# Optimization experiments

Hardware: AMD Instinct MI355X
Metric: run time of the kernel (lower is better)

## Reference

```python
import jax, jax.numpy as jnp
import numpy as np
import math

D_SINGLE, D_PAIR, H, PQ, PV = 384, 128, 12, 4, 8
DH = D_SINGLE // H
OUT_DIM = H * DH + H * PV * 4 + H * D_PAIR


def setup_inputs() -> dict:
    key = jax.random.key(0)
    ks = jax.random.split(key, 24)
    B, L = 1, 512
    inp = {
        'single': jax.random.normal(ks[0], (B, L, D_SINGLE), jnp.float32),
        'pair': jax.random.normal(ks[1], (B, L, L, D_PAIR), jnp.float32),
        'rot_mats': jax.random.normal(ks[2], (B, L, 3, 3), jnp.float32),
        'trans': jax.random.normal(ks[3], (B, L, 3), jnp.float32),
        'mask': jnp.ones((B, L), jnp.float32),
        'ln_w': jnp.ones((D_SINGLE,), jnp.float32),
        'ln_b': jnp.zeros((D_SINGLE,), jnp.float32),
        'Wq': jax.random.normal(ks[4], (D_SINGLE, H * DH), jnp.float32) * 0.02,
        'bq': jnp.zeros((H * DH,), jnp.float32),
        'Wk': jax.random.normal(ks[5], (D_SINGLE, H * DH), jnp.float32) * 0.02,
        'bk': jnp.zeros((H * DH,), jnp.float32),
        'Wv': jax.random.normal(ks[6], (D_SINGLE, H * DH), jnp.float32) * 0.02,
        'bv': jnp.zeros((H * DH,), jnp.float32),
        'Wqp': jax.random.normal(ks[7], (D_SINGLE, H * PQ * 3), jnp.float32) * 0.02,
        'bqp': jnp.zeros((H * PQ * 3,), jnp.float32),
        'Wkp': jax.random.normal(ks[8], (D_SINGLE, H * PQ * 3), jnp.float32) * 0.02,
        'bkp': jnp.zeros((H * PQ * 3,), jnp.float32),
        'Wvp': jax.random.normal(ks[9], (D_SINGLE, H * PV * 3), jnp.float32) * 0.02,
        'bvp': jnp.zeros((H * PV * 3,), jnp.float32),
        'Wpb': jax.random.normal(ks[10], (D_PAIR, H), jnp.float32) * 0.02,
        'bpb': jnp.zeros((H,), jnp.float32),
        'Wo': jax.random.normal(ks[11], (OUT_DIM, D_SINGLE), jnp.float32) * 0.02,
        'bo': jnp.zeros((D_SINGLE,), jnp.float32),
        'w_c': jnp.asarray(1.0 / math.sqrt(3.0), jnp.float32),
        'w_l': jnp.asarray(1.0 / 3.0, jnp.float32),
        'gamma_h': jnp.ones((H,), jnp.float32),
    }
    return inp


def _layer_norm(x, w, b, eps=1e-5):
    mu = jnp.mean(x, axis=-1, keepdims=True)
    var = jnp.mean((x - mu) ** 2, axis=-1, keepdims=True)
    return (x - mu) * jax.lax.rsqrt(var + eps) * w + b


def reference(single, pair, rot_mats, trans, mask, ln_w, ln_b, Wq, bq, Wk, bk, Wv, bv,
              Wqp, bqp, Wkp, bkp, Wvp, bvp, Wpb, bpb, Wo, bo, w_c, w_l, gamma_h):
    B, L, _ = single.shape
    sn = _layer_norm(single, ln_w, ln_b)
    q = (sn @ Wq + bq).reshape(B, L, H, DH)
    k = (sn @ Wk + bk).reshape(B, L, H, DH)
    v = (sn @ Wv + bv).reshape(B, L, H, DH)
    qp = (sn @ Wqp + bqp).reshape(B, L, H, PQ, 3)
    kp = (sn @ Wkp + bkp).reshape(B, L, H, PQ, 3)
    vp = (sn @ Wvp + bvp).reshape(B, L, H, PV, 3)

    t = trans[:, :, None, None, :]  # [B,L,1,1,3]
    qg = jnp.einsum('blij,blhpj->blhpi', rot_mats, qp) + t
    kg = jnp.einsum('blij,blhpj->blhpi', rot_mats, kp) + t
    vg = jnp.einsum('blij,blhpj->blhpi', rot_mats, vp) + t

    # sequence logits [B,H,L,L]
    seq_logits = jnp.einsum('bihd,bjhd->bhij', q, k) * w_c / math.sqrt(DH)

    # geometric logits: pairwise point distances [B,H,L,L]
    q_pts = jnp.transpose(qg, (0, 2, 1, 3, 4))  # [B,H,L,PQ,3]
    k_pts = jnp.transpose(kg, (0, 2, 1, 3, 4))
    diff = q_pts[:, :, :, None] - k_pts[:, :, None]  # [B,H,L,L,PQ,3]
    dist_sq = jnp.sum(diff ** 2, axis=-1)            # [B,H,L,L,PQ]
    geo_logits = -0.5 * jnp.sum(dist_sq, axis=-1) * gamma_h[None, :, None, None] * w_l

    pair_bias = jnp.transpose(pair @ Wpb + bpb, (0, 3, 1, 2))  # [B,H,L,L]
    logits = seq_logits + geo_logits + pair_bias

    mask_2d = (mask[:, :, None] * mask[:, None, :])[:, None]  # [B,1,L,L]
    logits = jnp.where(mask_2d > 0, logits, jnp.float32(-1e9))
    attn = jax.nn.softmax(logits, axis=-1)  # [B,H,L,L]

    # sequence aggregation -> [B,L,H,DH]
    seq_out = jnp.einsum('bhij,bjhd->bihd', attn, v).reshape(B, L, H * DH)

    # point aggregation -> local frame features
    pts_out = jnp.einsum('bhij,bjhpd->bihpd', attn, vg)  # [B,L,H,PV,3]
    pts_local = jnp.einsum('blji,blhpj->blhpi', rot_mats, pts_out - t)
    pts_norm = jnp.linalg.norm(pts_local, axis=-1, keepdims=True)
    pts_feat = jnp.concatenate([pts_norm, pts_local], axis=-1).reshape(B, L, H * PV * 4)

    # pair aggregation -> [B,L,H*D_PAIR]
    pair_out = jnp.einsum('bhij,bijd->bihd', attn, pair).reshape(B, L, H * D_PAIR)

    combined = jnp.concatenate([seq_out, pts_feat, pair_out], axis=-1)
    return combined @ Wo + bo
```

## Files before the change

kernel.cpp:

```cpp
#include <hip/hip_runtime.h>
#include <math.h>

#define LQ    512
#define DS    384
#define DPAIR 128
#define NH    12
#define NPP   1792
#define TJC   64
#define NC    8

typedef unsigned short u16;
typedef unsigned int   u32;
typedef __attribute__((ext_vector_type(8))) short bf16x8;
typedef __attribute__((ext_vector_type(4))) float f32x4;

__device__ inline u16 bf16_rne(float x) {
  u32 u = __float_as_uint(x);
  u32 r = (u + 0x7FFFu + ((u >> 16) & 1u)) >> 16;
  return (u16)r;
}
__device__ inline void split_bf16(float x, u16& h, u16& l) {
  u16 hb = bf16_rne(x);
  float hf = __uint_as_float(((u32)hb) << 16);
  h = hb;
  l = bf16_rne(x - hf);
}

__global__ __launch_bounds__(256) void k_prep(
    const float* __restrict__ Wq, const float* __restrict__ Wk,
    const float* __restrict__ Wv, const float* __restrict__ Wqp,
    const float* __restrict__ Wkp, const float* __restrict__ Wvp,
    const float* __restrict__ bq, const float* __restrict__ bk,
    const float* __restrict__ bv, const float* __restrict__ bqp,
    const float* __restrict__ bkp, const float* __restrict__ bvp,
    const float* __restrict__ Wpb, const float* __restrict__ Wo,
    const float* __restrict__ xs, const float* __restrict__ ln_w,
    const float* __restrict__ ln_b,
    u16* __restrict__ Wth, u16* __restrict__ Wtl,
    float* __restrict__ bcat, float* __restrict__ WpbT,
    u16* __restrict__ WoTh, u16* __restrict__ WoTl,
    u16* __restrict__ snh, u16* __restrict__ snl) {
  __shared__ u16 sh_hi[64][66], sh_lo[64][66];
  int blk = blockIdx.x, t = threadIdx.x;
  if (blk < 168) {
    int kb = blk / 28, cb = blk % 28;
    int k0 = kb * 64, c0 = cb * 64;
    for (int e = t; e < 4096; e += 256) {
      int rr = e >> 6, cc = e & 63;
      int k = k0 + rr, c = c0 + cc;
      float v = 0.f;
      if (c < 384)       v = Wq[k*384 + c];
      else if (c < 768)  v = Wk[k*384 + c-384];
      else if (c < 1152) v = Wv[k*384 + c-768];
      else if (c < 1296) v = Wqp[k*144 + c-1152];
      else if (c < 1440) v = Wkp[k*144 + c-1296];
      else if (c < 1728) v = Wvp[k*288 + c-1440];
      u16 h_, l_; split_bf16(v, h_, l_);
      sh_hi[rr][cc] = h_; sh_lo[rr][cc] = l_;
    }
    __syncthreads();
    for (int e = t; e < 4096; e += 256) {
      int cc = e >> 6, kk = e & 63;
      Wth[(size_t)(c0+cc)*DS + k0 + kk] = sh_hi[kk][cc];
      Wtl[(size_t)(c0+cc)*DS + k0 + kk] = sh_lo[kk][cc];
    }
  } else if (blk == 168) {
    for (int e = t; e < NPP + NH*DPAIR; e += 256) {
      if (e < NPP) {
        int c = e;
        float v = 0.f;
        if (c < 384)       v = bq[c];
        else if (c < 768)  v = bk[c-384];
        else if (c < 1152) v = bv[c-768];
        else if (c < 1296) v = bqp[c-1152];
        else if (c < 1440) v = bkp[c-1296];
        else if (c < 1728) v = bvp[c-1440];
        bcat[c] = v;
      } else {
        int e2 = e - NPP;
        int k = e2 / NH, h = e2 % NH;
        WpbT[h*DPAIR + k] = Wpb[e2];
      }
    }
  } else if (blk < 385) {
    int idx = blk - 169;
    int kt = idx % 36, nt = idx / 36;
    int k0 = kt * 64, n0 = nt * 64;
    for (int e = t; e < 4096; e += 256) {
      int rr = e >> 6, cc = e & 63;
      float v = Wo[(size_t)(k0+rr)*384 + n0 + cc];
      u16 h_, l_; split_bf16(v, h_, l_);
      sh_hi[rr][cc] = h_; sh_lo[rr][cc] = l_;
    }
    __syncthreads();
    for (int e = t; e < 4096; e += 256) {
      int cc = e >> 6, kk = e & 63;
      WoTh[(size_t)(n0+cc)*2304 + k0 + kk] = sh_hi[kk][cc];
      WoTl[(size_t)(n0+cc)*2304 + k0 + kk] = sh_lo[kk][cc];
    }
  } else {
    int i = blk - 385;
    float* red = (float*)&sh_hi[0][0];
    float a0 = xs[i*DS + t];
    float a1 = (t < 128) ? xs[i*DS + 256 + t] : 0.f;
    red[t] = a0 + a1; __syncthreads();
    for (int s = 128; s > 0; s >>= 1) { if (t < s) red[t] += red[t+s]; __syncthreads(); }
    float mu = red[0] * (1.f/384.f);
    __syncthreads();
    float d0 = a0 - mu, d1 = (t < 128) ? (a1 - mu) : 0.f;
    red[t] = d0*d0 + d1*d1; __syncthreads();
    for (int s = 128; s > 0; s >>= 1) { if (t < s) red[t] += red[t+s]; __syncthreads(); }
    float rstd = rsqrtf(red[0] * (1.f/384.f) + 1e-5f);
    u16 h_, l_;
    float y0 = d0*rstd*ln_w[t] + ln_b[t];
    split_bf16(y0, h_, l_); snh[i*DS + t] = h_; snl[i*DS + t] = l_;
    if (t < 128) {
      float y1 = d1*rstd*ln_w[256+t] + ln_b[256+t];
      split_bf16(y1, h_, l_); snh[i*DS + 256 + t] = h_; snl[i*DS + 256 + t] = l_;
    }
  }
}

__global__ __launch_bounds__(256) void k_gemm_mfma(
    const u16* __restrict__ Ah, const u16* __restrict__ Al,
    const u16* __restrict__ Bth, const u16* __restrict__ Btl,
    const float* __restrict__ bias, float* __restrict__ C,
    float* __restrict__ Cpart, int M, int N, int K) {
  int t = threadIdx.x;
  int lane = t & 63, wave = t >> 6;
  int wr = wave >> 1, wc = wave & 1;
  int i0 = blockIdx.y * 64 + wr * 32;
  int j0 = blockIdx.x * 64 + wc * 32;
  int KS = gridDim.z;
  int kper = K / KS;
  size_t kbeg = (size_t)blockIdx.z * kper;
  int lr = lane & 15, lk = (lane >> 4) << 3;

  const u16* a0h = Ah  + (size_t)(i0 + lr) * K + kbeg + lk;
  const u16* a1h = a0h + (size_t)16 * K;
  const u16* a0l = Al  + (size_t)(i0 + lr) * K + kbeg + lk;
  const u16* a1l = a0l + (size_t)16 * K;
  const u16* b0h = Bth + (size_t)(j0 + lr) * K + kbeg + lk;
  const u16* b1h = b0h + (size_t)16 * K;
  const u16* b0l = Btl + (size_t)(j0 + lr) * K + kbeg + lk;
  const u16* b1l = b0l + (size_t)16 * K;

  f32x4 c00 = {0.f,0.f,0.f,0.f}, c01 = c00, c10 = c00, c11 = c00;
  for (int k = 0; k < kper; k += 32) {
    bf16x8 A0h = *(const bf16x8*)(a0h + k);
    bf16x8 A1h = *(const bf16x8*)(a1h + k);
    bf16x8 B0h = *(const bf16x8*)(b0h + k);
    bf16x8 B1h = *(const bf16x8*)(b1h + k);
    bf16x8 A0l = *(const bf16x8*)(a0l + k);
    bf16x8 A1l = *(const bf16x8*)(a1l + k);
    bf16x8 B0l = *(const bf16x8*)(b0l + k);
    bf16x8 B1l = *(const bf16x8*)(b1l + k);
    c00 = __builtin_amdgcn_mfma_f32_16x16x32_bf16(A0h, B0h, c00, 0, 0, 0);
    c01 = __builtin_amdgcn_mfma_f32_16x16x32_bf16(A0h, B1h, c01, 0, 0, 0);
    c10 = __builtin_amdgcn_mfma_f32_16x16x32_bf16(A1h, B0h, c10, 0, 0, 0);
    c11 = __builtin_amdgcn_mfma_f32_16x16x32_bf16(A1h, B1h, c11, 0, 0, 0);
    c00 = __builtin_amdgcn_mfma_f32_16x16x32_bf16(A0h, B0l, c00, 0, 0, 0);
    c01 = __builtin_amdgcn_mfma_f32_16x16x32_bf16(A0h, B1l, c01, 0, 0, 0);
    c10 = __builtin_amdgcn_mfma_f32_16x16x32_bf16(A1h, B0l, c10, 0, 0, 0);
    c11 = __builtin_amdgcn_mfma_f32_16x16x32_bf16(A1h, B1l, c11, 0, 0, 0);
    c00 = __builtin_amdgcn_mfma_f32_16x16x32_bf16(A0l, B0h, c00, 0, 0, 0);
    c01 = __builtin_amdgcn_mfma_f32_16x16x32_bf16(A0l, B1h, c01, 0, 0, 0);
    c10 = __builtin_amdgcn_mfma_f32_16x16x32_bf16(A1l, B0h, c10, 0, 0, 0);
    c11 = __builtin_amdgcn_mfma_f32_16x16x32_bf16(A1l, B1h, c11, 0, 0, 0);
  }

  int orow = (lane >> 4) << 2;
  int col0 = j0 + lr, col1 = j0 + 16 + lr;
  if (KS == 1) {
    float bb0 = bias[col0], bb1 = bias[col1];
    #pragma unroll
    for (int r = 0; r < 4; r++) {
      int row0 = i0 + orow + r, row1 = row0 + 16;
      C[(size_t)row0*N + col0] = c00[r] + bb0;
      C[(size_t)row0*N + col1] = c01[r] + bb1;
      C[(size_t)row1*N + col0] = c10[r] + bb0;
      C[(size_t)row1*N + col1] = c11[r] + bb1;
    }
  } else {
    float* dst = Cpart + (size_t)blockIdx.z * M * N;
    #pragma unroll
    for (int r = 0; r < 4; r++) {
      int row0 = i0 + orow + r, row1 = row0 + 16;
      dst[(size_t)row0*N + col0] = c00[r];
      dst[(size_t)row0*N + col1] = c01[r];
      dst[(size_t)row1*N + col0] = c10[r];
      dst[(size_t)row1*N + col1] = c11[r];
    }
  }
}

__global__ void k_reduce_bias(const float* __restrict__ part, const float* __restrict__ bias,
                              float* __restrict__ out, int MN, int N, int KS) {
  int e = blockIdx.x * 256 + threadIdx.x;
  if (e >= MN) return;
  float s = bias[e % N];
  for (int z = 0; z < KS; z++) s += part[(size_t)z*MN + e];
  out[e] = s;
}

__global__ __launch_bounds__(256) void k_feat_logits(
    const float* __restrict__ C1, const float* __restrict__ rot,
    const float* __restrict__ trans, const float* __restrict__ gamma,
    const float* __restrict__ w_c, const float* __restrict__ w_l,
    float* __restrict__ S) {
  __shared__ u16 Ash[64][72], Asl[64][72], Bsh[64][72], Bsl[64][72];
  int h = blockIdx.z;
  int i0 = blockIdx.y * 64, j0 = blockIdx.x * 64;
  int t = threadIdx.x;

  if (t < 128) {
    int row = t & 63, side = t >> 6;
    int gi = (side ? j0 : i0) + row;
    float R[9], tr[3];
    #pragma unroll
    for (int r = 0; r < 9; r++) R[r] = rot[(size_t)gi*9 + r];
    #pragma unroll
    for (int r = 0; r < 3; r++) tr[r] = trans[(size_t)gi*3 + r];
    float sc = w_c[0] * rsqrtf(32.f);
    float gp = gamma[h] * w_l[0];
    u16 (*Fh)[72] = side ? Bsh : Ash;
    u16 (*Fl)[72] = side ? Bsl : Asl;
    const float* qk = C1 + (size_t)gi*NPP + (side ? 384 : 0) + h*32;
    u16 h_, l_;
    #pragma unroll 8
    for (int d = 0; d < 32; d++) {
      float v = side ? qk[d] : sc*qk[d];
      split_bf16(v, h_, l_); Fh[row][d] = h_; Fl[row][d] = l_;
    }
    const float* pp = C1 + (size_t)gi*NPP + (side ? 1296 : 1152) + h*12;
    float ss = 0.f;
    #pragma unroll
    for (int p = 0; p < 4; p++) {
      float x = pp[p*3], y = pp[p*3+1], z = pp[p*3+2];
      #pragma unroll
      for (int r = 0; r < 3; r++) {
        float g = fmaf(R[r*3],x, fmaf(R[r*3+1],y, fmaf(R[r*3+2],z, tr[r])));
        float v = side ? g : gp*g;
        split_bf16(v, h_, l_); Fh[row][32+p*3+r] = h_; Fl[row][32+p*3+r] = l_;
        ss = fmaf(g,g,ss);
      }
    }
    float c44 = side ? 1.f : -0.5f*gp*ss;
    float c45 = side ? -0.5f*gp*ss : 1.f;
    split_bf16(c44, h_, l_); Fh[row][44] = h_; Fl[row][44] = l_;
    split_bf16(c45, h_, l_); Fh[row][45] = h_; Fl[row][45] = l_;
    #pragma unroll
    for (int d = 46; d < 64; d++) { Fh[row][d] = 0; Fl[row][d] = 0; }
  }
  __syncthreads();

  int lane = t & 63, wave = t >> 6, wr = wave >> 1, wc = wave & 1;
  int lr = lane & 15, lk = (lane >> 4) << 3;
  f32x4 c00 = {0.f,0.f,0.f,0.f}, c01 = c00, c10 = c00, c11 = c00;
  #pragma unroll
  for (int ks = 0; ks < 64; ks += 32) {
    bf16x8 A0h = *(const bf16x8*)&Ash[wr*32 + lr][ks + lk];
    bf16x8 A1h = *(const bf16x8*)&Ash[wr*32 + 16 + lr][ks + lk];
    bf16x8 B0h = *(const bf16x8*)&Bsh[wc*32 + lr][ks + lk];
    bf16x8 B1h = *(const bf16x8*)&Bsh[wc*32 + 16 + lr][ks + lk];
    bf16x8 A0l = *(const bf16x8*)&Asl[wr*32 + lr][ks + lk];
    bf16x8 A1l = *(const bf16x8*)&Asl[wr*32 + 16 + lr][ks + lk];
    bf16x8 B0l = *(const bf16x8*)&Bsl[wc*32 + lr][ks + lk];
    bf16x8 B1l = *(const bf16x8*)&Bsl[wc*32 + 16 + lr][ks + lk];
    c00 = __builtin_amdgcn_mfma_f32_16x16x32_bf16(A0h, B0h, c00, 0, 0, 0);
    c01 = __builtin_amdgcn_mfma_f32_16x16x32_bf16(A0h, B1h, c01, 0, 0, 0);
    c10 = __builtin_amdgcn_mfma_f32_16x16x32_bf16(A1h, B0h, c10, 0, 0, 0);
    c11 = __builtin_amdgcn_mfma_f32_16x16x32_bf16(A1h, B1h, c11, 0, 0, 0);
    c00 = __builtin_amdgcn_mfma_f32_16x16x32_bf16(A0h, B0l, c00, 0, 0, 0);
    c01 = __builtin_amdgcn_mfma_f32_16x16x32_bf16(A0h, B1l, c01, 0, 0, 0);
    c10 = __builtin_amdgcn_mfma_f32_16x16x32_bf16(A1h, B0l, c10, 0, 0, 0);
    c11 = __builtin_amdgcn_mfma_f32_16x16x32_bf16(A1h, B1l, c11, 0, 0, 0);
    c00 = __builtin_amdgcn_mfma_f32_16x16x32_bf16(A0l, B0h, c00, 0, 0, 0);
    c01 = __builtin_amdgcn_mfma_f32_16x16x32_bf16(A0l, B1h, c01, 0, 0, 0);
    c10 = __builtin_amdgcn_mfma_f32_16x16x32_bf16(A1l, B0h, c10, 0, 0, 0);
    c11 = __builtin_amdgcn_mfma_f32_16x16x32_bf16(A1l, B1h, c11, 0, 0, 0);
  }

  int orow = (lane >> 4) << 2;
  int col0 = j0 + wc*32 + lr, col1 = col0 + 16;
  int rbase = i0 + wr*32 + orow;
  #pragma unroll
  for (int r = 0; r < 4; r++) {
    S[((size_t)h*LQ + rbase + r)*LQ + col0]      = c00[r];
    S[((size_t)h*LQ + rbase + r)*LQ + col1]      = c01[r];
    S[((size_t)h*LQ + rbase + 16 + r)*LQ + col0] = c10[r];
    S[((size_t)h*LQ + rbase + 16 + r)*LQ + col1] = c11[r];
  }
}

__global__ __launch_bounds__(256, 2) void k_pair_chunk(
    const float* __restrict__ pair, const float* __restrict__ WpbT,
    const float* __restrict__ bpb, const float* __restrict__ mask,
    float* __restrict__ S, float* __restrict__ pairpart, float* __restrict__ msum) {
  __shared__ float tile[TJC*133];
  __shared__ float wt[NH*TJC];
  int i = blockIdx.x, c = blockIdx.y, t = threadIdx.x;
  int j0 = c*TJC;

  const float4* src = (const float4*)(pair + ((size_t)i*LQ + j0)*DPAIR);
  #pragma unroll
  for (int u = 0; u < 8; u++) {
    int e = t + u*256; int row = e >> 5, c4 = e & 31;
    *(float4*)&tile[row*133 + c4*4] = src[e];
  }

  int j = t & 63;
  int hg = __builtin_amdgcn_readfirstlane(t >> 6);
  int h0 = hg*3;
  float l[3];
  #pragma unroll
  for (int q = 0; q < 3; q++)
    l[q] = S[((size_t)(h0+q)*LQ + i)*LQ + j0 + j] + bpb[h0+q];
  bool dead = (mask[i] * mask[j0 + j] <= 0.f);
  __syncthreads();

  {
    const float* w0p = WpbT + (size_t)(h0+0)*DPAIR;
    const float* w1p = WpbT + (size_t)(h0+1)*DPAIR;
    const float* w2p = WpbT + (size_t)(h0+2)*DPAIR;
    float a0 = 0.f, a1 = 0.f, a2 = 0.f;
    #pragma unroll 8
    for (int k = 0; k < DPAIR; k += 4) {
      float4 pv = *(const float4*)&tile[j*133 + k];
      float4 w0 = *(const float4*)(w0p + k);
      float4 w1 = *(const float4*)(w1p + k);
      float4 w2 = *(const float4*)(w2p + k);
      a0 = fmaf(pv.x,w0.x, fmaf(pv.y,w0.y, fmaf(pv.z,w0.z, fmaf(pv.w,w0.w, a0))));
      a1 = fmaf(pv.x,w1.x, fmaf(pv.y,w1.y, fmaf(pv.z,w1.z, fmaf(pv.w,w1.w, a1))));
      a2 = fmaf(pv.x,w2.x, fmaf(pv.y,w2.y, fmaf(pv.z,w2.z, fmaf(pv.w,w2.w, a2))));
    }
    l[0] += a0; l[1] += a1; l[2] += a2;
    if (dead) { l[0] = -1e9f; l[1] = -1e9f; l[2] = -1e9f; }
  }

  #pragma unroll
  for (int q = 0; q < 3; q++) {
    float m = l[q];
    #pragma unroll
    for (int o = 32; o > 0; o >>= 1) m = fmaxf(m, __shfl_xor(m, o, 64));
    float w = __expf(l[q] - m);
    float sm = w;
    #pragma unroll
    for (int o = 32; o > 0; o >>= 1) sm += __shfl_xor(sm, o, 64);
    wt[(h0+q)*TJC + j] = w;
    S[((size_t)(h0+q)*LQ + i)*LQ + j0 + j] = w;
    if (j == 0) {
      float* dst = msum + (((size_t)i*NC + c)*NH + h0 + q)*2;
      dst[0] = m; dst[1] = sm;
    }
  }
  __syncthreads();

  int dg = t & 31, strip = t >> 5, jb = strip*8;
  float4 pv[8];
  #pragma unroll
  for (int q = 0; q < 8; q++) pv[q] = *(const float4*)&tile[(jb+q)*133 + dg*4];
  float4 acc[NH];
  #pragma unroll
  for (int h = 0; h < NH; h++) acc[h] = make_float4(0.f,0.f,0.f,0.f);
  #pragma unroll
  for (int h = 0; h < NH; h++) {
    float4 w0 = *(const float4*)&wt[h*TJC + jb];
    float4 w1 = *(const float4*)&wt[h*TJC + jb + 4];
    float wq[8] = {w0.x,w0.y,w0.z,w0.w,w1.x,w1.y,w1.z,w1.w};
    float4 a = acc[h];
    #pragma unroll
    for (int q = 0; q < 8; q++) {
      a.x = fmaf(wq[q], pv[q].x, a.x);
      a.y = fmaf(wq[q], pv[q].y, a.y);
      a.z = fmaf(wq[q], pv[q].z, a.z);
      a.w = fmaf(wq[q], pv[q].w, a.w);
    }
    acc[h] = a;
  }
  __syncthreads();

  float4* red4 = (float4*)tile;
  float4 tot[2];
  tot[0] = make_float4(0.f,0.f,0.f,0.f);
  tot[1] = make_float4(0.f,0.f,0.f,0.f);
  #pragma unroll
  for (int half = 0; half < 2; half++) {
    if ((strip >> 2) == half) {
      #pragma unroll
      for (int h = 0; h < NH; h++)
        red4[(((strip & 3)*NH) + h)*32 + dg] = acc[h];
    }
    __syncthreads();
    for (int e = t, u = 0; e < NH*32; e += 256, u++) {
      int rh = e >> 5, rd = e & 31;
      #pragma unroll
      for (int s4 = 0; s4 < 4; s4++) {
        float4 v = red4[((s4*NH) + rh)*32 + rd];
        tot[u].x += v.x; tot[u].y += v.y; tot[u].z += v.z; tot[u].w += v.w;
      }
    }
    __syncthreads();
  }
  for (int e = t, u = 0; e < NH*32; e += 256, u++) {
    int rh = e >> 5, rd = e & 31;
    *(float4*)&pairpart[(((size_t)i*NC + c)*NH + rh)*DPAIR + rd*4] = tot[u];
  }
}

__global__ __launch_bounds__(256, 2) void k_attn_full(
    const float* __restrict__ S, const float* __restrict__ msum,
    const float* __restrict__ pairpart,
    const float* __restrict__ C1, const float* __restrict__ rot,
    const float* __restrict__ trans,
    u16* __restrict__ combh, u16* __restrict__ combl) {
  __shared__ u16 Ash[64][72], Asl[64][72], Vsh[64][72], Vsl[64][72];
  __shared__ float scs_l[64][NC];
  __shared__ float Of[64][66];
  int i0 = blockIdx.x * 64;
  int h = blockIdx.y;
  int t = threadIdx.x, lane = t & 63, wave = t >> 6, wr = wave >> 1, wc = wave & 1;
  int lr = lane & 15, lk = (lane >> 4) << 3;

  if (t < 64) {
    int gi = i0 + t;
    float mc[NC], sc[NC], m = -3.0e38f;
    #pragma unroll
    for (int c = 0; c < NC; c++) {
      const float* p = msum + (((size_t)gi*NC + c)*NH + h)*2;
      mc[c] = p[0]; sc[c] = p[1];
      m = fmaxf(m, mc[c]);
    }
    float den = 0.f;
    #pragma unroll
    for (int c = 0; c < NC; c++) den += sc[c] * __expf(mc[c] - m);
    float inv = 1.f / den;
    #pragma unroll
    for (int c = 0; c < NC; c++) scs_l[t][c] = __expf(mc[c] - m) * inv;
  }
  __syncthreads();

  for (int e = t; e < 64*DPAIR; e += 256) {
    int m = e >> 7, d = e & 127;
    float s = 0.f;
    #pragma unroll
    for (int c = 0; c < NC; c++)
      s = fmaf(scs_l[m][c], pairpart[(((size_t)(i0+m)*NC + c)*NH + h)*DPAIR + d], s);
    u16 h_, l_; split_bf16(s, h_, l_);
    size_t dst = (size_t)(i0+m)*2304 + 768 + h*DPAIR + d;
    combh[dst] = h_; combl[dst] = l_;
  }

  f32x4 c00 = {0.f,0.f,0.f,0.f}, c01 = c00, c10 = c00, c11 = c00;
  for (int jc = 0; jc < 8; jc++) {
    int j0 = jc * 64;
    for (int e = t; e < 4096; e += 256) {
      int m = e >> 6, j = e & 63;
      float w = S[((size_t)h*LQ + i0 + m)*LQ + j0 + j] * scs_l[m][jc];
      u16 h_, l_; split_bf16(w, h_, l_);
      Ash[m][j] = h_; Asl[m][j] = l_;
    }
    {
      int j = t & 63, ng = t >> 6;
      int gj = j0 + j;
      u16 h_, l_;
      if (ng < 2) {
        const float* vrow = C1 + (size_t)gj*NPP + 768 + h*32 + ng*16;
        #pragma unroll
        for (int q = 0; q < 16; q++) {
          split_bf16(vrow[q], h_, l_);
          Vsh[ng*16 + q][j] = h_; Vsl[ng*16 + q][j] = l_;
        }
      } else {
        const float* prow = C1 + (size_t)gj*NPP + 1440 + h*24;
        const float* R = rot + (size_t)gj*9;
        const float* tr = trans + (size_t)gj*3;
        int nbase = ng * 16;
        #pragma unroll
        for (int q = 0; q < 16; q++) {
          int n = nbase + q;
          float val = 0.f;
          if (n < 56) {
            int pp = (n - 32) / 3, rr = (n - 32) % 3;
            float x = prow[pp*3], y = prow[pp*3+1], z = prow[pp*3+2];
            val = fmaf(R[rr*3], x, fmaf(R[rr*3+1], y, fmaf(R[rr*3+2], z, tr[rr])));
          }
          split_bf16(val, h_, l_);
          Vsh[n][j] = h_; Vsl[n][j] = l_;
        }
      }
    }
    __syncthreads();
    #pragma unroll
    for (int ks = 0; ks < 64; ks += 32) {
      bf16x8 A0h = *(const bf16x8*)&Ash[wr*32 + lr][ks + lk];
      bf16x8 A1h = *(const bf16x8*)&Ash[wr*32 + 16 + lr][ks + lk];
      bf16x8 B0h = *(const bf16x8*)&Vsh[wc*32 + lr][ks + lk];
      bf16x8 B1h = *(const bf16x8*)&Vsh[wc*32 + 16 + lr][ks + lk];
      bf16x8 A0l = *(const bf16x8*)&Asl[wr*32 + lr][ks + lk];
      bf16x8 A1l = *(const bf16x8*)&Asl[wr*32 + 16 + lr][ks + lk];
      bf16x8 B0l = *(const bf16x8*)&Vsl[wc*32 + lr][ks + lk];
      bf16x8 B1l = *(const bf16x8*)&Vsl[wc*32 + 16 + lr][ks + lk];
      c00 = __builtin_amdgcn_mfma_f32_16x16x32_bf16(A0h, B0h, c00, 0, 0, 0);
      c01 = __builtin_amdgcn_mfma_f32_16x16x32_bf16(A0h, B1h, c01, 0, 0, 0);
      c10 = __builtin_amdgcn_mfma_f32_16x16x32_bf16(A1h, B0h, c10, 0, 0, 0);
      c11 = __builtin_amdgcn_mfma_f32_16x16x32_bf16(A1h, B1h, c11, 0, 0, 0);
      c00 = __builtin_amdgcn_mfma_f32_16x16x32_bf16(A0h, B0l, c00, 0, 0, 0);
      c01 = __builtin_amdgcn_mfma_f32_16x16x32_bf16(A0h, B1l, c01, 0, 0, 0);
      c10 = __builtin_amdgcn_mfma_f32_16x16x32_bf16(A1h, B0l, c10, 0, 0, 0);
      c11 = __builtin_amdgcn_mfma_f32_16x16x32_bf16(A1h, B1l, c11, 0, 0, 0);
      c00 = __builtin_amdgcn_mfma_f32_16x16x32_bf16(A0l, B0h, c00, 0, 0, 0);
      c01 = __builtin_amdgcn_mfma_f32_16x16x32_bf16(A0l, B1h, c01, 0, 0, 0);
      c10 = __builtin_amdgcn_mfma_f32_16x16x32_bf16(A1l, B0h, c10, 0, 0, 0);
      c11 = __builtin_amdgcn_mfma_f32_16x16x32_bf16(A1l, B1h, c11, 0, 0, 0);
    }
    __syncthreads();
  }

  int orow = (lane >> 4) << 2;
  #pragma unroll
  for (int r = 0; r < 4; r++) {
    Of[wr*32 + orow + r][wc*32 + lr]           = c00[r];
    Of[wr*32 + orow + r][wc*32 + 16 + lr]      = c01[r];
    Of[wr*32 + 16 + orow + r][wc*32 + lr]      = c10[r];
    Of[wr*32 + 16 + orow + r][wc*32 + 16 + lr] = c11[r];
  }
  __syncthreads();

  for (int e = t; e < 64*40; e += 256) {
    int w = e % 40, m = e / 40;
    int gi = i0 + m;
    u16 h_, l_;
    if (w < 32) {
      split_bf16(Of[m][w], h_, l_);
      combh[(size_t)gi*2304 + h*32 + w] = h_;
      combl[(size_t)gi*2304 + h*32 + w] = l_;
    } else {
      int pp = w - 32;
      float g0 = Of[m][32+pp*3], g1 = Of[m][32+pp*3+1], g2 = Of[m][32+pp*3+2];
      const float* R = rot + (size_t)gi*9;
      const float* tr = trans + (size_t)gi*3;
      float x = g0 - tr[0], y = g1 - tr[1], z = g2 - tr[2];
      float lx = fmaf(R[0],x, fmaf(R[3],y, R[6]*z));
      float ly = fmaf(R[1],x, fmaf(R[4],y, R[7]*z));
      float lz = fmaf(R[2],x, fmaf(R[5],y, R[8]*z));
      float nrm = sqrtf(fmaf(lx,lx, fmaf(ly,ly, lz*lz)));
      size_t dst = (size_t)gi*2304 + 384 + ((size_t)h*8 + pp)*4;
      split_bf16(nrm, h_, l_); combh[dst+0] = h_; combl[dst+0] = l_;
      split_bf16(lx,  h_, l_); combh[dst+1] = h_; combl[dst+1] = l_;
      split_bf16(ly,  h_, l_); combh[dst+2] = h_; combl[dst+2] = l_;
      split_bf16(lz,  h_, l_); combh[dst+3] = h_; combl[dst+3] = l_;
    }
  }
}

extern "C" void kernel_launch(void* const* d_in, const int* in_sizes, int n_in,
                              void* d_out, int out_size, void* d_ws, size_t ws_size,
                              hipStream_t stream) {
  const float* single = (const float*)d_in[0];
  const float* pair   = (const float*)d_in[1];
  const float* rot    = (const float*)d_in[2];
  const float* trans  = (const float*)d_in[3];
  const float* mask   = (const float*)d_in[4];
  const float* ln_w   = (const float*)d_in[5];
  const float* ln_b   = (const float*)d_in[6];
  const float* Wq     = (const float*)d_in[7];
  const float* bq     = (const float*)d_in[8];
  const float* Wk     = (const float*)d_in[9];
  const float* bk     = (const float*)d_in[10];
  const float* Wv     = (const float*)d_in[11];
  const float* bv     = (const float*)d_in[12];
  const float* Wqp    = (const float*)d_in[13];
  const float* bqp    = (const float*)d_in[14];
  const float* Wkp    = (const float*)d_in[15];
  const float* bkp    = (const float*)d_in[16];
  const float* Wvp    = (const float*)d_in[17];
  const float* bvp    = (const float*)d_in[18];
  const float* Wpb    = (const float*)d_in[19];
  const float* bpb    = (const float*)d_in[20];
  const float* Wo     = (const float*)d_in[21];
  const float* bo     = (const float*)d_in[22];
  const float* w_c    = (const float*)d_in[23];
  const float* w_l    = (const float*)d_in[24];
  const float* gamma  = (const float*)d_in[25];
  float* out = (float*)d_out;

  float* p = (float*)d_ws;
  auto alloc = [&](size_t n) { float* r = p; p += n; return r; };
  u16* WcatTh = (u16*)alloc((size_t)NPP*DS/2);
  u16* WcatTl = (u16*)alloc((size_t)NPP*DS/2);
  u16* snh    = (u16*)alloc((size_t)LQ*DS/2);
  u16* snl    = (u16*)alloc((size_t)LQ*DS/2);
  u16* WoTh   = (u16*)alloc((size_t)DS*2304/2);
  u16* WoTl   = (u16*)alloc((size_t)DS*2304/2);
  u16* combh  = (u16*)alloc((size_t)LQ*2304/2);
  u16* combl  = (u16*)alloc((size_t)LQ*2304/2);
  float* bcat    = alloc(NPP);
  float* WpbT    = alloc((size_t)NH*DPAIR);
  float* C1      = alloc((size_t)LQ*NPP);
  float* S       = alloc((size_t)NH*LQ*LQ);
  float* pairpart= alloc((size_t)LQ*NC*NH*DPAIR);
  float* msum    = alloc((size_t)LQ*NC*NH*2);
  float* outpart = alloc((size_t)8*LQ*DS);

  k_prep<<<dim3(897), 256, 0, stream>>>(
      Wq, Wk, Wv, Wqp, Wkp, Wvp, bq, bk, bv, bqp, bkp, bvp, Wpb, Wo,
      single, ln_w, ln_b, WcatTh, WcatTl, bcat, WpbT, WoTh, WoTl, snh, snl);
  k_gemm_mfma<<<dim3(NPP/64, LQ/64, 1), 256, 0, stream>>>(
      snh, snl, WcatTh, WcatTl, bcat, C1, nullptr, LQ, NPP, DS);
  k_feat_logits<<<dim3(LQ/64, LQ/64, NH), 256, 0, stream>>>(
      C1, rot, trans, gamma, w_c, w_l, S);
  k_pair_chunk<<<dim3(LQ, NC), 256, 0, stream>>>(pair, WpbT, bpb, mask, S, pairpart, msum);
  k_attn_full<<<dim3(LQ/64, NH), 256, 0, stream>>>(
      S, msum, pairpart, C1, rot, trans, combh, combl);
  k_gemm_mfma<<<dim3(DS/64, LQ/64, 8), 256, 0, stream>>>(
      combh, combl, WoTh, WoTl, nullptr, nullptr, outpart, LQ, DS, 2304);
  k_reduce_bias<<<dim3((LQ*DS + 255)/256), 256, 0, stream>>>(outpart, bo, out, LQ*DS, DS, 8);
}
```

Baseline: 373.8 us.

## Fuse pair chunks into one block per row with online softmax rescaling

The pair kernel now handles all eight j-chunks of a row in a single block. It keeps running-max accumulators rescaled online and register-prefetches the next chunk's pair tile while computing the current one. The block computes the per-chunk softmax scales itself and writes the normalized pair aggregation straight into the bf16 hi/lo combined buffer. This removes the pairpart/msum intermediates and the reduction in k_attn_full, but the grid drops from 4096 to 512 blocks, which lowers parallelism and raises register pressure with the launch-bounds occupancy hint removed.

```diff
diff --git a/kernel.cpp b/kernel.cpp
--- a/kernel.cpp
+++ b/kernel.cpp
@@ -293,92 +293,137 @@
   }
 }
 
-__global__ __launch_bounds__(256, 2) void k_pair_chunk(
+__global__ __launch_bounds__(256) void k_pair(
     const float* __restrict__ pair, const float* __restrict__ WpbT,
     const float* __restrict__ bpb, const float* __restrict__ mask,
-    float* __restrict__ S, float* __restrict__ pairpart, float* __restrict__ msum) {
+    float* S, float* __restrict__ scs_g,
+    u16* __restrict__ combh, u16* __restrict__ combl) {
   __shared__ float tile[TJC*133];
   __shared__ float wt[NH*TJC];
-  int i = blockIdx.x, c = blockIdx.y, t = threadIdx.x;
-  int j0 = c*TJC;
-
-  const float4* src = (const float4*)(pair + ((size_t)i*LQ + j0)*DPAIR);
+  __shared__ float msc[NC][NH], ssc[NC][NH];
+  __shared__ float rfac[NH], dinv[NH];
+  int i = blockIdx.x, t = threadIdx.x;
+  int j = t & 63;
+  int hg = t >> 6;
+  int h0 = hg * 3;
+  int dg = t & 31, strip = t >> 5, jb = strip*8;
+
+  float b0 = bpb[h0], b1 = bpb[h0+1], b2 = bpb[h0+2];
+  float mi = mask[i];
+  const float* w0p = WpbT + (size_t)(h0+0)*DPAIR;
+  const float* w1p = WpbT + (size_t)(h0+1)*DPAIR;
+  const float* w2p = WpbT + (size_t)(h0+2)*DPAIR;
+
+  float4 acc[NH];
+  #pragma unroll
+  for (int h = 0; h < NH; h++) acc[h] = make_float4(0.f,0.f,0.f,0.f);
+  float mrun[3] = {-3.0e38f, -3.0e38f, -3.0e38f};
+
+  float4 pf[8];
+  {
+    const float4* src = (const float4*)(pair + (size_t)i*LQ*DPAIR);
+    #pragma unroll
+    for (int u = 0; u < 8; u++) pf[u] = src[t + u*256];
+  }
   #pragma unroll
   for (int u = 0; u < 8; u++) {
     int e = t + u*256; int row = e >> 5, c4 = e & 31;
-    *(float4*)&tile[row*133 + c4*4] = src[e];
-  }
-
-  int j = t & 63;
-  int hg = __builtin_amdgcn_readfirstlane(t >> 6);
-  int h0 = hg*3;
-  float l[3];
-  #pragma unroll
-  for (int q = 0; q < 3; q++)
-    l[q] = S[((size_t)(h0+q)*LQ + i)*LQ + j0 + j] + bpb[h0+q];
-  bool dead = (mask[i] * mask[j0 + j] <= 0.f);
+    *(float4*)&tile[row*133 + c4*4] = pf[u];
+  }
   __syncthreads();
 
-  {
-    const float* w0p = WpbT + (size_t)(h0+0)*DPAIR;
-    const float* w1p = WpbT + (size_t)(h0+1)*DPAIR;
-    const float* w2p = WpbT + (size_t)(h0+2)*DPAIR;
-    float a0 = 0.f, a1 = 0.f, a2 = 0.f;
-    #pragma unroll 8
-    for (int k = 0; k < DPAIR; k += 4) {
-      float4 pv = *(const float4*)&tile[j*133 + k];
-      float4 w0 = *(const float4*)(w0p + k);
-      float4 w1 = *(const float4*)(w1p + k);
-      float4 w2 = *(const float4*)(w2p + k);
-      a0 = fmaf(pv.x,w0.x, fmaf(pv.y,w0.y, fmaf(pv.z,w0.z, fmaf(pv.w,w0.w, a0))));
-      a1 = fmaf(pv.x,w1.x, fmaf(pv.y,w1.y, fmaf(pv.z,w1.z, fmaf(pv.w,w1.w, a1))));
-      a2 = fmaf(pv.x,w2.x, fmaf(pv.y,w2.y, fmaf(pv.z,w2.z, fmaf(pv.w,w2.w, a2))));
-    }
-    l[0] += a0; l[1] += a1; l[2] += a2;
-    if (dead) { l[0] = -1e9f; l[1] = -1e9f; l[2] = -1e9f; }
-  }
-
-  #pragma unroll
-  for (int q = 0; q < 3; q++) {
-    float m = l[q];
-    #pragma unroll
-    for (int o = 32; o > 0; o >>= 1) m = fmaxf(m, __shfl_xor(m, o, 64));
-    float w = __expf(l[q] - m);
-    float sm = w;
-    #pragma unroll
-    for (int o = 32; o > 0; o >>= 1) sm += __shfl_xor(sm, o, 64);
-    wt[(h0+q)*TJC + j] = w;
-    S[((size_t)(h0+q)*LQ + i)*LQ + j0 + j] = w;
-    if (j == 0) {
-      float* dst = msum + (((size_t)i*NC + c)*NH + h0 + q)*2;
-      dst[0] = m; dst[1] = sm;
-    }
-  }
-  __syncthreads();
-
-  int dg = t & 31, strip = t >> 5, jb = strip*8;
-  float4 pv[8];
-  #pragma unroll
-  for (int q = 0; q < 8; q++) pv[q] = *(const float4*)&tile[(jb+q)*133 + dg*4];
-  float4 acc[NH];
-  #pragma unroll
-  for (int h = 0; h < NH; h++) acc[h] = make_float4(0.f,0.f,0.f,0.f);
-  #pragma unroll
-  for (int h = 0; h < NH; h++) {
-    float4 w0 = *(const float4*)&wt[h*TJC + jb];
-    float4 w1 = *(const float4*)&wt[h*TJC + jb + 4];
-    float wq[8] = {w0.x,w0.y,w0.z,w0.w,w1.x,w1.y,w1.z,w1.w};
-    float4 a = acc[h];
-    #pragma unroll
-    for (int q = 0; q < 8; q++) {
-      a.x = fmaf(wq[q], pv[q].x, a.x);
-      a.y = fmaf(wq[q], pv[q].y, a.y);
-      a.z = fmaf(wq[q], pv[q].z, a.z);
-      a.w = fmaf(wq[q], pv[q].w, a.w);
-    }
-    acc[h] = a;
-  }
-  __syncthreads();
+  for (int c = 0; c < NC; c++) {
+    if (c < NC-1) {
+      const float4* src = (const float4*)(pair + ((size_t)i*LQ + (c+1)*TJC)*DPAIR);
+      #pragma unroll
+      for (int u = 0; u < 8; u++) pf[u] = src[t + u*256];
+    }
+    int j0 = c*TJC;
+    float l0 = S[((size_t)(h0+0)*LQ + i)*LQ + j0 + j] + b0;
+    float l1 = S[((size_t)(h0+1)*LQ + i)*LQ + j0 + j] + b1;
+    float l2 = S[((size_t)(h0+2)*LQ + i)*LQ + j0 + j] + b2;
+    {
+      float a0 = 0.f, a1 = 0.f, a2 = 0.f;
+      #pragma unroll 8
+      for (int k = 0; k < DPAIR; k += 4) {
+        float4 pv = *(const float4*)&tile[j*133 + k];
+        float4 w0 = *(const float4*)(w0p + k);
+        float4 w1 = *(const float4*)(w1p + k);
+        float4 w2 = *(const float4*)(w2p + k);
+        a0 = fmaf(pv.x,w0.x, fmaf(pv.y,w0.y, fmaf(pv.z,w0.z, fmaf(pv.w,w0.w, a0))));
+        a1 = fmaf(pv.x,w1.x, fmaf(pv.y,w1.y, fmaf(pv.z,w1.z, fmaf(pv.w,w1.w, a1))));
+        a2 = fmaf(pv.x,w2.x, fmaf(pv.y,w2.y, fmaf(pv.z,w2.z, fmaf(pv.w,w2.w, a2))));
+      }
+      l0 += a0; l1 += a1; l2 += a2;
+      bool dead = (mi * mask[j0 + j] <= 0.f);
+      if (dead) { l0 = -1e9f; l1 = -1e9f; l2 = -1e9f; }
+    }
+    #pragma unroll
+    for (int q = 0; q < 3; q++) {
+      float lv = (q==0) ? l0 : (q==1) ? l1 : l2;
+      float m = lv;
+      #pragma unroll
+      for (int o = 32; o > 0; o >>= 1) m = fmaxf(m, __shfl_xor(m, o, 64));
+      float w = __expf(lv - m);
+      float sm = w;
+      #pragma unroll
+      for (int o = 32; o > 0; o >>= 1) sm += __shfl_xor(sm, o, 64);
+      float mnew = fmaxf(mrun[q], m);
+      float f  = __expf(m - mnew);
+      float rf = __expf(mrun[q] - mnew);
+      mrun[q] = mnew;
+      wt[(h0+q)*TJC + j] = w * f;
+      S[((size_t)(h0+q)*LQ + i)*LQ + j0 + j] = w;
+      if (j == 0) { msc[c][h0+q] = m; ssc[c][h0+q] = sm; rfac[h0+q] = rf; }
+    }
+    __syncthreads();
+    {
+      float4 pv[8];
+      #pragma unroll
+      for (int q = 0; q < 8; q++) pv[q] = *(const float4*)&tile[(jb+q)*133 + dg*4];
+      #pragma unroll
+      for (int h = 0; h < NH; h++) {
+        float rf = rfac[h];
+        float4 w0 = *(const float4*)&wt[h*TJC + jb];
+        float4 w1 = *(const float4*)&wt[h*TJC + jb + 4];
+        float wq[8] = {w0.x,w0.y,w0.z,w0.w,w1.x,w1.y,w1.z,w1.w};
+        float4 a = acc[h];
+        a.x *= rf; a.y *= rf; a.z *= rf; a.w *= rf;
+        #pragma unroll
+        for (int q = 0; q < 8; q++) {
+          a.x = fmaf(wq[q], pv[q].x, a.x);
+          a.y = fmaf(wq[q], pv[q].y, a.y);
+          a.z = fmaf(wq[q], pv[q].z, a.z);
+          a.w = fmaf(wq[q], pv[q].w, a.w);
+        }
+        acc[h] = a;
+      }
+    }
+    __syncthreads();
+    if (c < NC-1) {
+      #pragma unroll
+      for (int u = 0; u < 8; u++) {
+        int e = t + u*256; int row = e >> 5, c4 = e & 31;
+        *(float4*)&tile[row*133 + c4*4] = pf[u];
+      }
+      __syncthreads();
+    }
+  }
+
+  if (j == 0) {
+    #pragma unroll
+    for (int q = 0; q < 3; q++) {
+      float M = mrun[q];
+      float den = 0.f;
+      #pragma unroll
+      for (int c = 0; c < NC; c++) den += ssc[c][h0+q] * __expf(msc[c][h0+q] - M);
+      float inv = 1.f / den;
+      dinv[h0+q] = inv;
+      #pragma unroll
+      for (int c = 0; c < NC; c++)
+        scs_g[((size_t)i*NH + h0+q)*NC + c] = __expf(msc[c][h0+q] - M) * inv;
+    }
+  }
 
   float4* red4 = (float4*)tile;
   float4 tot[2];
@@ -404,13 +449,18 @@
   }
   for (int e = t, u = 0; e < NH*32; e += 256, u++) {
     int rh = e >> 5, rd = e & 31;
-    *(float4*)&pairpart[(((size_t)i*NC + c)*NH + rh)*DPAIR + rd*4] = tot[u];
+    float inv = dinv[rh];
+    size_t dst = (size_t)i*2304 + 768 + rh*DPAIR + rd*4;
+    u16 h_, l_;
+    split_bf16(tot[u].x * inv, h_, l_); combh[dst+0] = h_; combl[dst+0] = l_;
+    split_bf16(tot[u].y * inv, h_, l_); combh[dst+1] = h_; combl[dst+1] = l_;
+    split_bf16(tot[u].z * inv, h_, l_); combh[dst+2] = h_; combl[dst+2] = l_;
+    split_bf16(tot[u].w * inv, h_, l_); combh[dst+3] = h_; combl[dst+3] = l_;
   }
 }
 
 __global__ __launch_bounds__(256, 2) void k_attn_full(
-    const float* __restrict__ S, const float* __restrict__ msum,
-    const float* __restrict__ pairpart,
+    const float* __restrict__ S, const float* __restrict__ scs_g,
     const float* __restrict__ C1, const float* __restrict__ rot,
     const float* __restrict__ trans,
     u16* __restrict__ combh, u16* __restrict__ combl) {
@@ -423,33 +473,11 @@
   int lr = lane & 15, lk = (lane >> 4) << 3;
 
   if (t < 64) {
-    int gi = i0 + t;
-    float mc[NC], sc[NC], m = -3.0e38f;
-    #pragma unroll
-    for (int c = 0; c < NC; c++) {
-      const float* p = msum + (((size_t)gi*NC + c)*NH + h)*2;
-      mc[c] = p[0]; sc[c] = p[1];
-      m = fmaxf(m, mc[c]);
-    }
-    float den = 0.f;
-    #pragma unroll
-    for (int c = 0; c < NC; c++) den += sc[c] * __expf(mc[c] - m);
-    float inv = 1.f / den;
-    #pragma unroll
-    for (int c = 0; c < NC; c++) scs_l[t][c] = __expf(mc[c] - m) * inv;
+    #pragma unroll
+    for (int c = 0; c < NC; c++)
+      scs_l[t][c] = scs_g[((size_t)(i0+t)*NH + h)*NC + c];
   }
   __syncthreads();
-
-  for (int e = t; e < 64*DPAIR; e += 256) {
-    int m = e >> 7, d = e & 127;
-    float s = 0.f;
-    #pragma unroll
-    for (int c = 0; c < NC; c++)
-      s = fmaf(scs_l[m][c], pairpart[(((size_t)(i0+m)*NC + c)*NH + h)*DPAIR + d], s);
-    u16 h_, l_; split_bf16(s, h_, l_);
-    size_t dst = (size_t)(i0+m)*2304 + 768 + h*DPAIR + d;
-    combh[dst] = h_; combl[dst] = l_;
-  }
 
   f32x4 c00 = {0.f,0.f,0.f,0.f}, c01 = c00, c10 = c00, c11 = c00;
   for (int jc = 0; jc < 8; jc++) {
@@ -599,8 +627,7 @@
   float* WpbT    = alloc((size_t)NH*DPAIR);
   float* C1      = alloc((size_t)LQ*NPP);
   float* S       = alloc((size_t)NH*LQ*LQ);
-  float* pairpart= alloc((size_t)LQ*NC*NH*DPAIR);
-  float* msum    = alloc((size_t)LQ*NC*NH*2);
+  float* scs_g   = alloc((size_t)LQ*NH*NC);
   float* outpart = alloc((size_t)8*LQ*DS);
 
   k_prep<<<dim3(897), 256, 0, stream>>>(
@@ -610,9 +637,10 @@
       snh, snl, WcatTh, WcatTl, bcat, C1, nullptr, LQ, NPP, DS);
   k_feat_logits<<<dim3(LQ/64, LQ/64, NH), 256, 0, stream>>>(
       C1, rot, trans, gamma, w_c, w_l, S);
-  k_pair_chunk<<<dim3(LQ, NC), 256, 0, stream>>>(pair, WpbT, bpb, mask, S, pairpart, msum);
+  k_pair<<<dim3(LQ), 256, 0, stream>>>(
+      pair, WpbT, bpb, mask, S, scs_g, combh, combl);
   k_attn_full<<<dim3(LQ/64, NH), 256, 0, stream>>>(
-      S, msum, pairpart, C1, rot, trans, combh, combl);
+      S, scs_g, C1, rot, trans, combh, combl);
   k_gemm_mfma<<<dim3(DS/64, LQ/64, 8), 256, 0, stream>>>(
       combh, combl, WoTh, WoTl, nullptr, nullptr, outpart, LQ, DS, 2304);
   k_reduce_bias<<<dim3((LQ*DS + 255)/256), 256, 0, stream>>>(outpart, bo, out, LQ*DS, DS, 8);
```

Result: slower. 421.0 us (+12.6%).
